# Performance work log

Hardware: AMD Instinct MI355X
Metric: run time of the kernel (lower is better)

## Reference

```python
import jax, jax.numpy as jnp
import numpy as np

NUM_HEADS = 16
NUM_KV_HEADS = 4
HEAD_DIM = 128
LAYER_IDX = 5
MASK_VALUE = -65504.0  # torch.finfo(torch.float16).min


def setup_inputs() -> dict:
    key = jax.random.key(0)
    ks = jax.random.split(key, 7)
    B, S, H = 2, 2048, 2048
    hidden_states = jax.random.normal(ks[0], (B, S, H), dtype=jnp.float32)
    k = jax.random.normal(ks[1], (B, NUM_KV_HEADS, S, HEAD_DIM), dtype=jnp.float32)
    v = jax.random.normal(ks[2], (B, NUM_KV_HEADS, S, HEAD_DIM), dtype=jnp.float32)
    std = 0.02
    w_q = jax.random.normal(ks[3], (H, H), dtype=jnp.float32) * std
    b_q = jnp.zeros((H,), dtype=jnp.float32)
    w_proj = jax.random.normal(ks[4], (H, H), dtype=jnp.float32) * (std / np.sqrt(2 * 24))
    b_proj = jnp.zeros((H,), dtype=jnp.float32)
    return {"hidden_states": hidden_states, "key": k, "value": v,
            "w_q": w_q, "b_q": b_q, "w_proj": w_proj, "b_proj": b_proj}


def reference(hidden_states, key, value, w_q, b_q, w_proj, b_proj):
    B, S, H = hidden_states.shape
    G = NUM_HEADS // NUM_KV_HEADS  # query heads per kv head
    dtype = hidden_states.dtype

    # query projection -> [B, kv_heads, group, S, head_dim]
    q = hidden_states @ w_q.T + b_q
    q = q.reshape(B, S, NUM_KV_HEADS, G, HEAD_DIM).transpose(0, 2, 3, 1, 4)

    # bigcode-style fp32 softmax with layer-wise unscale
    unscale = float(LAYER_IDX + 1)  # scale_attention_softmax_in_fp32 and upcast
    scale_factor = (1.0 / unscale) * (HEAD_DIM ** -0.5)  # scale_attn_weights

    # scores: [B, kv_heads, group, S_q, S_k]
    scores = jnp.einsum('bkgsd,bktd->bkgst', q, key) * scale_factor

    causal = jnp.tril(jnp.ones((S, S), dtype=bool))  # [S_q, S_k]
    scores = jnp.where(causal, scores, jnp.asarray(MASK_VALUE, dtype=scores.dtype))

    probs = jax.nn.softmax((scores * unscale).astype(jnp.float32), axis=-1).astype(dtype)

    out = jnp.einsum('bkgst,bktd->bkgsd', probs, value)
    out = out.transpose(0, 3, 1, 2, 4).reshape(B, S, H)
    out = out @ w_proj.T + b_proj
    return out
```

## Files before the change

### kernel.cpp

```cpp
#include <hip/hip_runtime.h>
#include <math.h>


#define RSQ128 0.08838834764831845
#define LOG2E  1.4426950408889634
#define RS2L   ((float)(RSQ128 * LOG2E))
#define CAP2   24.0f

typedef __attribute__((ext_vector_type(8))) short short8;
typedef __attribute__((ext_vector_type(4))) float f32x4;
typedef __attribute__((ext_vector_type(16))) float f32x16;

static __device__ __forceinline__ unsigned short f2bf(float x) {
    union { float f; unsigned u; } v; v.f = x;
    unsigned r = v.u + 0x7FFFu + ((v.u >> 16) & 1u);
    return (unsigned short)(r >> 16);
}

static __device__ __forceinline__ unsigned pack_bf16(float lo, float hi) {
#if __has_builtin(__builtin_amdgcn_cvt_pk_bf16_f32)
    return __builtin_bit_cast(unsigned, __builtin_amdgcn_cvt_pk_bf16_f32(lo, hi));
#else
    return (unsigned)f2bf(lo) | ((unsigned)f2bf(hi) << 16);
#endif
}

static __device__ __forceinline__ float fexp2(float x) {
#if __has_builtin(__builtin_amdgcn_exp2f)
    return __builtin_amdgcn_exp2f(x);
#else
    return exp2f(x);
#endif
}

static __device__ __forceinline__ void gl_lds16(const void* g, void* l) {
    __builtin_amdgcn_global_load_lds(
        (const __attribute__((address_space(1))) void*)g,
        (__attribute__((address_space(3))) void*)l, 16, 0, 0);
}

static __device__ __forceinline__ void cvt8(const float* __restrict__ in,
                                            unsigned short* __restrict__ out,
                                            int i) {
    const float4 a = *(const float4*)(in + i);
    const float4 b = *(const float4*)(in + i + 4);
    short8 o;
    o[0] = (short)f2bf(a.x); o[1] = (short)f2bf(a.y);
    o[2] = (short)f2bf(a.z); o[3] = (short)f2bf(a.w);
    o[4] = (short)f2bf(b.x); o[5] = (short)f2bf(b.y);
    o[6] = (short)f2bf(b.z); o[7] = (short)f2bf(b.w);
    *(short8*)(out + i) = o;
}

__global__ void prep_all(const float* __restrict__ hs, unsigned short* __restrict__ hsb,
                         const float* __restrict__ wq, unsigned short* __restrict__ wqb,
                         const float* __restrict__ K,  unsigned short* __restrict__ Kpk,
                         const float* __restrict__ V,  unsigned short* __restrict__ Vpk)
{
    __shared__ float Ts[32][132];
    const int bid = blockIdx.x, tid = threadIdx.x;

    if (bid < 4096) {
        cvt8(hs, hsb, (bid * 256 + tid) * 8);
        return;
    }
    if (bid < 6144) {
        cvt8(wq, wqb, ((bid - 4096) * 256 + tid) * 8);
        return;
    }
    if (bid < 6656) {
        const int idx = bid - 6144;
        const int t = idx & 63, bkh = idx >> 6;
        const float* src = K + ((size_t)bkh * 2048 + t * 32) * 128;
        unsigned short* dst = Kpk + ((size_t)bkh * 64 + t) * 4096;
#pragma unroll
        for (int p = 0; p < 2; ++p) {
            const int g = p * 256 + tid;
            const int ch = g >> 5, key = g & 31;
            const float4 a = *(const float4*)(src + key * 128 + ch * 8);
            const float4 b = *(const float4*)(src + key * 128 + ch * 8 + 4);
            short8 o;
            o[0] = (short)f2bf(a.x); o[1] = (short)f2bf(a.y);
            o[2] = (short)f2bf(a.z); o[3] = (short)f2bf(a.w);
            o[4] = (short)f2bf(b.x); o[5] = (short)f2bf(b.y);
            o[6] = (short)f2bf(b.z); o[7] = (short)f2bf(b.w);
            *(short8*)(dst + ch * 256 + key * 8) = o;
        }
        return;
    }
    {
        const int idx = bid - 6656;
        const int t = idx & 63, bkh = idx >> 6;
        const float* src = V + ((size_t)bkh * 2048 + t * 32) * 128;
        unsigned short* dst = Vpk + ((size_t)bkh * 64 + t) * 4096;
#pragma unroll
        for (int p = 0; p < 4; ++p) {
            const int g = p * 256 + tid;
            const int key = g >> 5, cq = g & 31;
            const float4 v = *(const float4*)(src + key * 128 + cq * 4);
            *(float4*)&Ts[key][cq * 4] = v;
        }
        __syncthreads();
#pragma unroll
        for (int p = 0; p < 2; ++p) {
            const int g = p * 256 + tid;
            const int kc = g >> 7, d = g & 127;
            short8 o;
#pragma unroll
            for (int j = 0; j < 8; ++j) o[j] = (short)f2bf(Ts[kc * 8 + j][d]);
            *(short8*)(dst + kc * 1024 + d * 8) = o;
        }
    }
}

template <int OMODE>
__global__ __launch_bounds__(512, 2) void gemm_nt_sk(
    const unsigned short* __restrict__ A,
    const unsigned short* __restrict__ W,
    const float* __restrict__ bias,
    void* __restrict__ Cout, int M, int N, int K, float oscale)
{
    __shared__ __align__(16) unsigned short SMEM[32768];
    unsigned short* Asb = SMEM;
    unsigned short* Wsb = SMEM + 16384;

    const int tid = threadIdx.x;
    const int g = tid >> 8;
    const int t2 = tid & 255;
    const int lane = tid & 63;
    const int wq = (tid >> 6) & 3;
    const int wm = wq & 1, wn = wq >> 1;
    const int m0 = blockIdx.y * 128, n0 = blockIdx.x * 128;
    const int r0 = t2 >> 2, c0 = t2 & 3;
    const int Kh = K >> 1;

    const unsigned short* Ag = A + (size_t)(m0 + r0) * K + g * Kh + c0 * 8;
    const unsigned short* Wg = W + (size_t)(n0 + r0) * K + g * Kh + c0 * 8;

    f32x4 acc[4][4];
#pragma unroll
    for (int i = 0; i < 4; ++i)
#pragma unroll
        for (int j = 0; j < 4; ++j) acc[i][j] = (f32x4){0.f, 0.f, 0.f, 0.f};

    const int lm = lane & 15, lk = (lane >> 4) * 8;
    unsigned short* As0 = Asb + g * 8192;
    unsigned short* Ws0 = Wsb + g * 8192;

    gl_lds16(Ag,                  As0 + t2 * 8);
    gl_lds16(Ag + (size_t)64 * K, As0 + (t2 + 256) * 8);
    gl_lds16(Wg,                  Ws0 + t2 * 8);
    gl_lds16(Wg + (size_t)64 * K, Ws0 + (t2 + 256) * 8);

    int buf = 0;
    for (int k0 = 0; k0 < Kh; k0 += 32) {
        __syncthreads();
        const int kn = k0 + 32;
        if (kn < Kh) {
            unsigned short* Ad = As0 + (buf ^ 1) * 4096;
            unsigned short* Wd = Ws0 + (buf ^ 1) * 4096;
            gl_lds16(Ag + kn,                  Ad + t2 * 8);
            gl_lds16(Ag + (size_t)64 * K + kn, Ad + (t2 + 256) * 8);
            gl_lds16(Wg + kn,                  Wd + t2 * 8);
            gl_lds16(Wg + (size_t)64 * K + kn, Wd + (t2 + 256) * 8);
        }

        const unsigned short* Ar = As0 + buf * 4096;
        const unsigned short* Wr = Ws0 + buf * 4096;
        short8 a[4], b[4];
#pragma unroll
        for (int i = 0; i < 4; ++i)
            a[i] = *(const short8*)&Ar[(64 * wm + 16 * i + lm) * 32 + lk];
#pragma unroll
        for (int j = 0; j < 4; ++j)
            b[j] = *(const short8*)&Wr[(64 * wn + 16 * j + lm) * 32 + lk];
#pragma unroll
        for (int i = 0; i < 4; ++i)
#pragma unroll
            for (int j = 0; j < 4; ++j)
                acc[i][j] = __builtin_amdgcn_mfma_f32_16x16x32_bf16(a[i], b[j], acc[i][j], 0, 0, 0);
        buf ^= 1;
    }

    float* MRG = (float*)SMEM;
    __syncthreads();
    if (g == 1) {
#pragma unroll
        for (int i = 0; i < 4; ++i)
#pragma unroll
            for (int j = 0; j < 4; ++j) {
                float4 v4;
                v4.x = acc[i][j][0]; v4.y = acc[i][j][1];
                v4.z = acc[i][j][2]; v4.w = acc[i][j][3];
                *(float4*)&MRG[((i * 4 + j) * 256 + wq * 64 + lane) * 4] = v4;
            }
    }
    __syncthreads();
    if (g == 0) {
        float bv[4];
#pragma unroll
        for (int j = 0; j < 4; ++j) bv[j] = bias[n0 + 64 * wn + 16 * j + lm];
#pragma unroll
        for (int i = 0; i < 4; ++i)
#pragma unroll
            for (int j = 0; j < 4; ++j) {
                const float4 v4 = *(const float4*)&MRG[((i * 4 + j) * 256 + wq * 64 + lane) * 4];
                const float s[4] = {v4.x, v4.y, v4.z, v4.w};
#pragma unroll
                for (int reg = 0; reg < 4; ++reg) {
                    const int row = m0 + 64 * wm + 16 * i + 4 * (lane >> 4) + reg;
                    const int col = n0 + 64 * wn + 16 * j + lm;
                    const float v = (acc[i][j][reg] + s[reg] + bv[j]) * oscale;
                    if (OMODE == 0) {
                        ((float*)Cout)[(size_t)row * N + col] = v;
                    } else {
                        const int bb = row >> 11, ss = row & 2047;
                        const int hh = col >> 7, dd = col & 127;
                        const size_t o = (size_t)((bb * 16 + hh) * 64 + (ss >> 5)) * 4096
                                       + (dd >> 3) * 256 + (ss & 31) * 8 + (dd & 7);
                        ((unsigned short*)Cout)[o] = f2bf(v);
                    }
                }
            }
    }
}

__global__ __launch_bounds__(128, 3) void attn_mfma12(
    const unsigned short* __restrict__ Qpk,
    const unsigned short* __restrict__ Kpk,
    const unsigned short* __restrict__ Vpk,
    unsigned short* __restrict__ O,
    const float* __restrict__ wp,
    unsigned short* __restrict__ wpb)
{
    __shared__ __align__(16) float MRG[4096];
    __shared__ float Lsm[64];

    const int tid = threadIdx.x;

    if (blockIdx.x >= 2048) {
        const int i = ((blockIdx.x - 2048) * 128 + tid) * 8;
        cvt8(wp, wpb, i);
        return;
    }

    const int lane = tid & 63, pz = tid >> 6;
    const int h2 = lane >> 5, ln = lane & 31;

    const int bid = blockIdx.x;
    const int grp = bid & 7;
    const int idx = bid >> 3;
    const int b = grp >> 2, kh = grp & 3;
    const int hl = idx & 3;
    const int qt = 63 - (idx >> 2);
    const int h = kh * 4 + hl;

    const unsigned short* Kbase = Kpk + (size_t)(b * 4 + kh) * 64 * 4096;
    const unsigned short* Vbase = Vpk + (size_t)(b * 4 + kh) * 64 * 4096;
    const int koff = h2 * 256 + ln * 8;
    const int voff = h2 * 1024 + ln * 8;

    unsigned short* QL = (unsigned short*)MRG;
    {
        const unsigned short* qsrc = Qpk + (size_t)((b * 16 + h) * 64 + qt) * 4096;
#pragma unroll
        for (int i = 0; i < 4; ++i)
            gl_lds16(qsrc + (i * 128 + tid) * 8, QL + (i * 128 + pz * 64) * 8);
    }

    f32x16 Ot[4];
#pragma unroll
    for (int mt = 0; mt < 4; ++mt)
#pragma unroll
        for (int r = 0; r < 16; ++r) Ot[mt][r] = 0.f;
    float l_ = 0.f;

    __syncthreads();

    const int q_lo = qt * 32;
    const int qg = q_lo + ln;
    const int q_hi = q_lo + 31;
    const int jmax = qt >> 1;

    for (int j = 0; j <= jmax; ++j) {
        const int t0 = 64 * j + 32 * pz;
        if (t0 > q_hi) continue;

        const unsigned short* Kt = Kbase + (size_t)(2 * j + pz) * 4096;
        const unsigned short* Vt = Vbase + (size_t)(2 * j + pz) * 4096;

        short8 kf[8], vf[8];
#pragma unroll
        for (int ks = 0; ks < 8; ++ks)
            kf[ks] = *(const short8*)(Kt + ks * 512 + koff);
#pragma unroll
        for (int i = 0; i < 8; ++i)
            vf[i] = *(const short8*)(Vt + (i >> 2) * 2048 + (i & 3) * 256 + voff);

        f32x16 St;
#pragma unroll
        for (int r = 0; r < 16; ++r) St[r] = 0.f;
#pragma unroll
        for (int ks = 0; ks < 8; ++ks) {
            const short8 qf = *(const short8*)(QL + ks * 512 + h2 * 256 + ln * 8);
            St = __builtin_amdgcn_mfma_f32_32x32x16_bf16(kf[ks], qf, St, 0, 0, 0);
        }

        float s_loc = 0.f;
        unsigned Pp[8];
        if (t0 + 31 <= q_lo) {
#pragma unroll
            for (int p = 0; p < 8; ++p) {
                const float p0 = fexp2(St[2 * p] - CAP2);
                const float p1 = fexp2(St[2 * p + 1] - CAP2);
                s_loc += p0 + p1;
                Pp[p] = pack_bf16(p0, p1);
            }
        } else {
#pragma unroll
            for (int p = 0; p < 8; ++p) {
                const int k0 = t0 + (2 * p & 3) + 8 * (2 * p >> 2) + 4 * h2;
                const int k1 = t0 + ((2 * p + 1) & 3) + 8 * ((2 * p + 1) >> 2) + 4 * h2;
                const float p0 = (k0 <= qg) ? fexp2(St[2 * p] - CAP2) : 0.f;
                const float p1 = (k1 <= qg) ? fexp2(St[2 * p + 1] - CAP2) : 0.f;
                s_loc += p0 + p1;
                Pp[p] = pack_bf16(p0, p1);
            }
        }
        s_loc += __shfl_xor(s_loc, 32);
        l_ += s_loc;

#pragma unroll
        for (int ks4 = 0; ks4 < 2; ++ks4) {
            const unsigned pa = Pp[4 * ks4 + 0], pb = Pp[4 * ks4 + 1];
            const unsigned pc = Pp[4 * ks4 + 2], pd = Pp[4 * ks4 + 3];
            const unsigned x0 = (unsigned)__shfl_xor((int)(h2 ? pa : pc), 32);
            const unsigned x1 = (unsigned)__shfl_xor((int)(h2 ? pb : pd), 32);
            union { unsigned u[4]; short8 s8; } fr;
            fr.u[0] = h2 ? x0 : pa;
            fr.u[1] = h2 ? x1 : pb;
            fr.u[2] = h2 ? pc : x0;
            fr.u[3] = h2 ? pd : x1;
#pragma unroll
            for (int mt = 0; mt < 4; ++mt)
                Ot[mt] = __builtin_amdgcn_mfma_f32_32x32x16_bf16(vf[ks4 * 4 + mt], fr.s8, Ot[mt], 0, 0, 0);
        }
    }

    __syncthreads();
    if (pz == 1) {
#pragma unroll
        for (int mt = 0; mt < 4; ++mt)
#pragma unroll
            for (int g = 0; g < 4; ++g) {
                float4 v4;
                v4.x = Ot[mt][4 * g + 0]; v4.y = Ot[mt][4 * g + 1];
                v4.z = Ot[mt][4 * g + 2]; v4.w = Ot[mt][4 * g + 3];
                *(float4*)&MRG[lane * 64 + (((mt * 4 + g + lane) & 15) * 4)] = v4;
            }
        Lsm[lane] = l_;
    }
    __syncthreads();
    if (pz == 0) {
        l_ += Lsm[lane];
#pragma unroll
        for (int mt = 0; mt < 4; ++mt)
#pragma unroll
            for (int g = 0; g < 4; ++g) {
                const float4 v4 = *(const float4*)&MRG[lane * 64 + (((mt * 4 + g + lane) & 15) * 4)];
                Ot[mt][4 * g + 0] += v4.x;
                Ot[mt][4 * g + 1] += v4.y;
                Ot[mt][4 * g + 2] += v4.z;
                Ot[mt][4 * g + 3] += v4.w;
            }
    }
    __syncthreads();

    if (pz == 0) {
        unsigned short* Es = (unsigned short*)MRG;
        const float inv = 1.0f / l_;
#pragma unroll
        for (int mt = 0; mt < 4; ++mt)
#pragma unroll
            for (int g = 0; g < 4; ++g) {
                uint2 pk;
                pk.x = pack_bf16(Ot[mt][4 * g + 0] * inv, Ot[mt][4 * g + 1] * inv);
                pk.y = pack_bf16(Ot[mt][4 * g + 2] * inv, Ot[mt][4 * g + 3] * inv);
                const int chunk = (4 * mt + g) ^ (ln & 15);
                *(uint2*)&Es[ln * 128 + chunk * 8 + 4 * h2] = pk;
            }
    }
    __syncthreads();
    if (pz == 0) {
        unsigned short* Es = (unsigned short*)MRG;
#pragma unroll
        for (int pp = 0; pp < 8; ++pp) {
            const int f = pp * 64 + lane;
            const int q = f >> 4, c = f & 15;
            const short8 v = *(const short8*)&Es[q * 128 + ((c ^ (q & 15)) * 8)];
            *(short8*)(O + (size_t)(b * 2048 + q_lo + q) * 2048 + h * 128 + c * 8) = v;
        }
    }
}

extern "C" void kernel_launch(void* const* d_in, const int* in_sizes, int n_in,
                              void* d_out, int out_size, void* d_ws, size_t ws_size,
                              hipStream_t stream) {
    const float* hs = (const float*)d_in[0];
    const float* k  = (const float*)d_in[1];
    const float* v  = (const float*)d_in[2];
    const float* wq = (const float*)d_in[3];
    const float* bq = (const float*)d_in[4];
    const float* wp = (const float*)d_in[5];
    const float* bp = (const float*)d_in[6];
    float* out = (float*)d_out;

    unsigned short* hsb  = (unsigned short*)d_ws;
    unsigned short* wqb  = hsb  + 8388608;
    unsigned short* kpk  = wqb  + 4194304;
    unsigned short* vpk  = kpk  + 2097152;
    unsigned short* qbuf = vpk  + 2097152;
    unsigned short* abuf = qbuf + 8388608;
    unsigned short* wpb  = hsb;

    prep_all<<<7168, 256, 0, stream>>>(hs, hsb, wq, wqb, k, kpk, v, vpk);

    dim3 gG(16, 32);
    gemm_nt_sk<2><<<gG, 512, 0, stream>>>(hsb, wqb, bq, qbuf, 4096, 2048, 2048, RS2L);
    attn_mfma12<<<6144, 128, 0, stream>>>(qbuf, kpk, vpk, abuf, wp, wpb);
    gemm_nt_sk<0><<<gG, 512, 0, stream>>>(abuf, wpb, bp, out, 4096, 2048, 2048, 1.0f);
}
```

Measured before the change: 265.8 us.

## Process two query heads per attention block to reuse K/V fragment loads

Each attention block now handles two query heads of the same KV group instead of one, halving the number of attention blocks. K and V fragments loaded from global memory are reused across both heads' QK and PV MFMAs, cutting K/V load traffic per unit of work. This doubles the output accumulators per thread, so launch bounds drop from 3 to 2 blocks per SM. The epilogue is factored into a macro and run once per head, which raises register pressure and serialises two LDS reductions.

Measured after the change: 271.6 us. 2.1% more time.

```diff
diff --git a/kernel.cpp b/kernel.cpp
--- a/kernel.cpp
+++ b/kernel.cpp
@@ -225,7 +225,63 @@
     }
 }
 
-__global__ __launch_bounds__(128, 3) void attn_mfma12(
+
+#define EPILOGUE(OTX, LX, HX)                                                   \
+    __syncthreads();                                                            \
+    if (pz == 1) {                                                              \
+        _Pragma("unroll")                                                       \
+        for (int mt = 0; mt < 4; ++mt)                                          \
+            _Pragma("unroll")                                                   \
+            for (int g = 0; g < 4; ++g) {                                       \
+                float4 v4;                                                      \
+                v4.x = OTX[mt][4 * g + 0]; v4.y = OTX[mt][4 * g + 1];           \
+                v4.z = OTX[mt][4 * g + 2]; v4.w = OTX[mt][4 * g + 3];           \
+                *(float4*)&MRG[lane * 64 + (((mt * 4 + g + lane) & 15) * 4)] = v4; \
+            }                                                                   \
+        Lsm[lane] = LX;                                                         \
+    }                                                                           \
+    __syncthreads();                                                            \
+    if (pz == 0) {                                                              \
+        LX += Lsm[lane];                                                        \
+        _Pragma("unroll")                                                       \
+        for (int mt = 0; mt < 4; ++mt)                                          \
+            _Pragma("unroll")                                                   \
+            for (int g = 0; g < 4; ++g) {                                       \
+                const float4 v4 = *(const float4*)&MRG[lane * 64 + (((mt * 4 + g + lane) & 15) * 4)]; \
+                OTX[mt][4 * g + 0] += v4.x;                                     \
+                OTX[mt][4 * g + 1] += v4.y;                                     \
+                OTX[mt][4 * g + 2] += v4.z;                                     \
+                OTX[mt][4 * g + 3] += v4.w;                                     \
+            }                                                                   \
+    }                                                                           \
+    __syncthreads();                                                            \
+    if (pz == 0) {                                                              \
+        unsigned short* Es = (unsigned short*)MRG;                              \
+        const float inv = 1.0f / LX;                                            \
+        _Pragma("unroll")                                                       \
+        for (int mt = 0; mt < 4; ++mt)                                          \
+            _Pragma("unroll")                                                   \
+            for (int g = 0; g < 4; ++g) {                                       \
+                uint2 pk;                                                       \
+                pk.x = pack_bf16(OTX[mt][4 * g + 0] * inv, OTX[mt][4 * g + 1] * inv); \
+                pk.y = pack_bf16(OTX[mt][4 * g + 2] * inv, OTX[mt][4 * g + 3] * inv); \
+                const int chunk = (4 * mt + g) ^ (ln & 15);                     \
+                *(uint2*)&Es[ln * 128 + chunk * 8 + 4 * h2] = pk;               \
+            }                                                                   \
+    }                                                                           \
+    __syncthreads();                                                            \
+    if (pz == 0) {                                                              \
+        unsigned short* Es = (unsigned short*)MRG;                              \
+        _Pragma("unroll")                                                       \
+        for (int pp = 0; pp < 8; ++pp) {                                        \
+            const int f = pp * 64 + lane;                                       \
+            const int q = f >> 4, c = f & 15;                                   \
+            const short8 v = *(const short8*)&Es[q * 128 + ((c ^ (q & 15)) * 8)]; \
+            *(short8*)(O + (size_t)(b * 2048 + q_lo + q) * 2048 + (HX) * 128 + c * 8) = v; \
+        }                                                                       \
+    }
+
+__global__ __launch_bounds__(128, 2) void attn_mfma13(
     const unsigned short* __restrict__ Qpk,
     const unsigned short* __restrict__ Kpk,
     const unsigned short* __restrict__ Vpk,
@@ -238,8 +294,8 @@
 
     const int tid = threadIdx.x;
 
-    if (blockIdx.x >= 2048) {
-        const int i = ((blockIdx.x - 2048) * 128 + tid) * 8;
+    if (blockIdx.x >= 1024) {
+        const int i = ((blockIdx.x - 1024) * 128 + tid) * 8;
         cvt8(wp, wpb, i);
         return;
     }
@@ -251,9 +307,9 @@
     const int grp = bid & 7;
     const int idx = bid >> 3;
     const int b = grp >> 2, kh = grp & 3;
-    const int hl = idx & 3;
-    const int qt = 63 - (idx >> 2);
-    const int h = kh * 4 + hl;
+    const int hp = idx & 1;
+    const int qt = 63 - (idx >> 1);
+    const int h0 = kh * 4 + 2 * hp;
 
     const unsigned short* Kbase = Kpk + (size_t)(b * 4 + kh) * 64 * 4096;
     const unsigned short* Vbase = Vpk + (size_t)(b * 4 + kh) * 64 * 4096;
@@ -261,19 +317,20 @@
     const int voff = h2 * 1024 + ln * 8;
 
     unsigned short* QL = (unsigned short*)MRG;
-    {
-        const unsigned short* qsrc = Qpk + (size_t)((b * 16 + h) * 64 + qt) * 4096;
+#pragma unroll
+    for (int ht = 0; ht < 2; ++ht) {
+        const unsigned short* qsrc = Qpk + (size_t)((b * 16 + h0 + ht) * 64 + qt) * 4096;
 #pragma unroll
         for (int i = 0; i < 4; ++i)
-            gl_lds16(qsrc + (i * 128 + tid) * 8, QL + (i * 128 + pz * 64) * 8);
-    }
-
-    f32x16 Ot[4];
+            gl_lds16(qsrc + (i * 128 + tid) * 8, QL + ht * 4096 + (i * 128 + pz * 64) * 8);
+    }
+
+    f32x16 Ot0[4], Ot1[4];
 #pragma unroll
     for (int mt = 0; mt < 4; ++mt)
 #pragma unroll
-        for (int r = 0; r < 16; ++r) Ot[mt][r] = 0.f;
-    float l_ = 0.f;
+        for (int r = 0; r < 16; ++r) { Ot0[mt][r] = 0.f; Ot1[mt][r] = 0.f; }
+    float l0 = 0.f, l1 = 0.f;
 
     __syncthreads();
 
@@ -289,13 +346,10 @@
         const unsigned short* Kt = Kbase + (size_t)(2 * j + pz) * 4096;
         const unsigned short* Vt = Vbase + (size_t)(2 * j + pz) * 4096;
 
-        short8 kf[8], vf[8];
+        short8 kf[8];
 #pragma unroll
         for (int ks = 0; ks < 8; ++ks)
             kf[ks] = *(const short8*)(Kt + ks * 512 + koff);
-#pragma unroll
-        for (int i = 0; i < 8; ++i)
-            vf[i] = *(const short8*)(Vt + (i >> 2) * 2048 + (i & 3) * 256 + voff);
 
         f32x16 St;
 #pragma unroll
@@ -306,15 +360,22 @@
             St = __builtin_amdgcn_mfma_f32_32x32x16_bf16(kf[ks], qf, St, 0, 0, 0);
         }
 
-        float s_loc = 0.f;
-        unsigned Pp[8];
-        if (t0 + 31 <= q_lo) {
+        short8 vf[8];
+#pragma unroll
+        for (int i = 0; i < 8; ++i)
+            vf[i] = *(const short8*)(Vt + (i >> 2) * 2048 + (i & 3) * 256 + voff);
+
+        const bool unmasked = (t0 + 31 <= q_lo);
+
+        float s0 = 0.f;
+        unsigned Pp0[8];
+        if (unmasked) {
 #pragma unroll
             for (int p = 0; p < 8; ++p) {
                 const float p0 = fexp2(St[2 * p] - CAP2);
                 const float p1 = fexp2(St[2 * p + 1] - CAP2);
-                s_loc += p0 + p1;
-                Pp[p] = pack_bf16(p0, p1);
+                s0 += p0 + p1;
+                Pp0[p] = pack_bf16(p0, p1);
             }
         } else {
 #pragma unroll
@@ -323,84 +384,80 @@
                 const int k1 = t0 + ((2 * p + 1) & 3) + 8 * ((2 * p + 1) >> 2) + 4 * h2;
                 const float p0 = (k0 <= qg) ? fexp2(St[2 * p] - CAP2) : 0.f;
                 const float p1 = (k1 <= qg) ? fexp2(St[2 * p + 1] - CAP2) : 0.f;
-                s_loc += p0 + p1;
-                Pp[p] = pack_bf16(p0, p1);
-            }
-        }
-        s_loc += __shfl_xor(s_loc, 32);
-        l_ += s_loc;
+                s0 += p0 + p1;
+                Pp0[p] = pack_bf16(p0, p1);
+            }
+        }
+        s0 += __shfl_xor(s0, 32);
+        l0 += s0;
+
+#pragma unroll
+        for (int r = 0; r < 16; ++r) St[r] = 0.f;
+#pragma unroll
+        for (int ks = 0; ks < 8; ++ks) {
+            const short8 qf = *(const short8*)(QL + 4096 + ks * 512 + h2 * 256 + ln * 8);
+            St = __builtin_amdgcn_mfma_f32_32x32x16_bf16(kf[ks], qf, St, 0, 0, 0);
+        }
+
+        float s1 = 0.f;
+        unsigned Pp1[8];
+        if (unmasked) {
+#pragma unroll
+            for (int p = 0; p < 8; ++p) {
+                const float p0 = fexp2(St[2 * p] - CAP2);
+                const float p1 = fexp2(St[2 * p + 1] - CAP2);
+                s1 += p0 + p1;
+                Pp1[p] = pack_bf16(p0, p1);
+            }
+        } else {
+#pragma unroll
+            for (int p = 0; p < 8; ++p) {
+                const int k0 = t0 + (2 * p & 3) + 8 * (2 * p >> 2) + 4 * h2;
+                const int k1 = t0 + ((2 * p + 1) & 3) + 8 * ((2 * p + 1) >> 2) + 4 * h2;
+                const float p0 = (k0 <= qg) ? fexp2(St[2 * p] - CAP2) : 0.f;
+                const float p1 = (k1 <= qg) ? fexp2(St[2 * p + 1] - CAP2) : 0.f;
+                s1 += p0 + p1;
+                Pp1[p] = pack_bf16(p0, p1);
+            }
+        }
+        s1 += __shfl_xor(s1, 32);
+        l1 += s1;
 
 #pragma unroll
         for (int ks4 = 0; ks4 < 2; ++ks4) {
-            const unsigned pa = Pp[4 * ks4 + 0], pb = Pp[4 * ks4 + 1];
-            const unsigned pc = Pp[4 * ks4 + 2], pd = Pp[4 * ks4 + 3];
-            const unsigned x0 = (unsigned)__shfl_xor((int)(h2 ? pa : pc), 32);
-            const unsigned x1 = (unsigned)__shfl_xor((int)(h2 ? pb : pd), 32);
-            union { unsigned u[4]; short8 s8; } fr;
-            fr.u[0] = h2 ? x0 : pa;
-            fr.u[1] = h2 ? x1 : pb;
-            fr.u[2] = h2 ? pc : x0;
-            fr.u[3] = h2 ? pd : x1;
-#pragma unroll
-            for (int mt = 0; mt < 4; ++mt)
-                Ot[mt] = __builtin_amdgcn_mfma_f32_32x32x16_bf16(vf[ks4 * 4 + mt], fr.s8, Ot[mt], 0, 0, 0);
-        }
-    }
-
-    __syncthreads();
-    if (pz == 1) {
-#pragma unroll
-        for (int mt = 0; mt < 4; ++mt)
-#pragma unroll
-            for (int g = 0; g < 4; ++g) {
-                float4 v4;
-                v4.x = Ot[mt][4 * g + 0]; v4.y = Ot[mt][4 * g + 1];
-                v4.z = Ot[mt][4 * g + 2]; v4.w = Ot[mt][4 * g + 3];
-                *(float4*)&MRG[lane * 64 + (((mt * 4 + g + lane) & 15) * 4)] = v4;
-            }
-        Lsm[lane] = l_;
-    }
-    __syncthreads();
-    if (pz == 0) {
-        l_ += Lsm[lane];
-#pragma unroll
-        for (int mt = 0; mt < 4; ++mt)
-#pragma unroll
-            for (int g = 0; g < 4; ++g) {
-                const float4 v4 = *(const float4*)&MRG[lane * 64 + (((mt * 4 + g + lane) & 15) * 4)];
-                Ot[mt][4 * g + 0] += v4.x;
-                Ot[mt][4 * g + 1] += v4.y;
-                Ot[mt][4 * g + 2] += v4.z;
-                Ot[mt][4 * g + 3] += v4.w;
-            }
-    }
-    __syncthreads();
-
-    if (pz == 0) {
-        unsigned short* Es = (unsigned short*)MRG;
-        const float inv = 1.0f / l_;
-#pragma unroll
-        for (int mt = 0; mt < 4; ++mt)
-#pragma unroll
-            for (int g = 0; g < 4; ++g) {
-                uint2 pk;
-                pk.x = pack_bf16(Ot[mt][4 * g + 0] * inv, Ot[mt][4 * g + 1] * inv);
-                pk.y = pack_bf16(Ot[mt][4 * g + 2] * inv, Ot[mt][4 * g + 3] * inv);
-                const int chunk = (4 * mt + g) ^ (ln & 15);
-                *(uint2*)&Es[ln * 128 + chunk * 8 + 4 * h2] = pk;
-            }
-    }
-    __syncthreads();
-    if (pz == 0) {
-        unsigned short* Es = (unsigned short*)MRG;
-#pragma unroll
-        for (int pp = 0; pp < 8; ++pp) {
-            const int f = pp * 64 + lane;
-            const int q = f >> 4, c = f & 15;
-            const short8 v = *(const short8*)&Es[q * 128 + ((c ^ (q & 15)) * 8)];
-            *(short8*)(O + (size_t)(b * 2048 + q_lo + q) * 2048 + h * 128 + c * 8) = v;
-        }
-    }
+            {
+                const unsigned pa = Pp0[4 * ks4 + 0], pb = Pp0[4 * ks4 + 1];
+                const unsigned pc = Pp0[4 * ks4 + 2], pd = Pp0[4 * ks4 + 3];
+                const unsigned x0 = (unsigned)__shfl_xor((int)(h2 ? pa : pc), 32);
+                const unsigned x1 = (unsigned)__shfl_xor((int)(h2 ? pb : pd), 32);
+                union { unsigned u[4]; short8 s8; } fr;
+                fr.u[0] = h2 ? x0 : pa;
+                fr.u[1] = h2 ? x1 : pb;
+                fr.u[2] = h2 ? pc : x0;
+                fr.u[3] = h2 ? pd : x1;
+#pragma unroll
+                for (int mt = 0; mt < 4; ++mt)
+                    Ot0[mt] = __builtin_amdgcn_mfma_f32_32x32x16_bf16(vf[ks4 * 4 + mt], fr.s8, Ot0[mt], 0, 0, 0);
+            }
+            {
+                const unsigned pa = Pp1[4 * ks4 + 0], pb = Pp1[4 * ks4 + 1];
+                const unsigned pc = Pp1[4 * ks4 + 2], pd = Pp1[4 * ks4 + 3];
+                const unsigned x0 = (unsigned)__shfl_xor((int)(h2 ? pa : pc), 32);
+                const unsigned x1 = (unsigned)__shfl_xor((int)(h2 ? pb : pd), 32);
+                union { unsigned u[4]; short8 s8; } fr;
+                fr.u[0] = h2 ? x0 : pa;
+                fr.u[1] = h2 ? x1 : pb;
+                fr.u[2] = h2 ? pc : x0;
+                fr.u[3] = h2 ? pd : x1;
+#pragma unroll
+                for (int mt = 0; mt < 4; ++mt)
+                    Ot1[mt] = __builtin_amdgcn_mfma_f32_32x32x16_bf16(vf[ks4 * 4 + mt], fr.s8, Ot1[mt], 0, 0, 0);
+            }
+        }
+    }
+
+    EPILOGUE(Ot0, l0, h0)
+    EPILOGUE(Ot1, l1, h0 + 1)
 }
 
 extern "C" void kernel_launch(void* const* d_in, const int* in_sizes, int n_in,
@@ -427,6 +484,6 @@
 
     dim3 gG(16, 32);
     gemm_nt_sk<2><<<gG, 512, 0, stream>>>(hsb, wqb, bq, qbuf, 4096, 2048, 2048, RS2L);
-    attn_mfma12<<<6144, 128, 0, stream>>>(qbuf, kpk, vpk, abuf, wp, wpb);
+    attn_mfma13<<<5120, 128, 0, stream>>>(qbuf, kpk, vpk, abuf, wp, wpb);
     gemm_nt_sk<0><<<gG, 512, 0, stream>>>(abuf, wpb, bp, out, 4096, 2048, 2048, 1.0f);
 }
```
